# Kernel tuning notes

Hardware: AMD Instinct MI355X
Metric: run time of the kernel (lower is better)

Reference implementation:

```python
import jax, jax.numpy as jnp
import numpy as np

D_KQ = 1024  # output_key_query_dim, used for the 1/sqrt(d) scale


def setup_inputs() -> dict:
    key = jax.random.key(0)
    kx, kq, kk, kv = jax.random.split(key, 4)
    B, S, D = 4, 2048, 1024
    x = jax.random.normal(kx, (B, S, D), dtype=jnp.float32)
    # nn.Linear(in, out, bias=False) weights, shape (out, in); y = x @ W.T
    scale = 1.0 / np.sqrt(D)
    Wq = jax.random.normal(kq, (D_KQ, D), dtype=jnp.float32) * scale
    Wk = jax.random.normal(kk, (D_KQ, D), dtype=jnp.float32) * scale
    Wv = jax.random.normal(kv, (D, D), dtype=jnp.float32) * scale
    return {"x": x, "Wq": Wq, "Wk": Wk, "Wv": Wv}


def reference(x, Wq, Wk, Wv):
    # q, k, v projections (bias=False): y = x @ W.T
    q = jnp.einsum('bsd,ed->bse', x, Wq)  # [B,S,Dkq]
    k = jnp.einsum('bsd,ed->bse', x, Wk)  # [B,S,Dkq]
    v = jnp.einsum('bsd,ed->bse', x, Wv)  # [B,S,Dv]
    scores = jnp.einsum('bqe,bke->bqk', q, k) / jnp.sqrt(
        jnp.asarray(D_KQ, dtype=q.dtype))
    # NOTE: the original torch code's masked_fill(causal_mask == 1, -inf) is a
    # no-op because the buffer contains only {-inf, 0} values, never 1.
    # Faithfully, NO causal mask is applied.
    attn = jax.nn.softmax(scores, axis=-1)
    # dropout in eval mode -> identity
    out = jnp.einsum('bqk,bke->bqe', attn, v)  # [B,S,Dv]
    return out
```

## Files before the change

### kernel.cpp

```cpp
#include <hip/hip_runtime.h>
#include <stdint.h>

#define B_ 4
#define S_ 2048
#define D_ 1024

typedef __attribute__((ext_vector_type(8))) short short8;
typedef __attribute__((ext_vector_type(4))) float f32x4;
typedef __attribute__((ext_vector_type(4))) int int4v;

__device__ inline ushort f2bf(float f) {
  union { float f; uint32_t u; } v; v.f = f;
  uint32_t u = v.u;
  u += 0x7FFFu + ((u >> 16) & 1u);
  return (ushort)(u >> 16);
}

__device__ inline void gload_lds16(const ushort* g, ushort* l) {
  __builtin_amdgcn_global_load_lds(
      (__attribute__((address_space(1))) void*)(uintptr_t)g,
      (__attribute__((address_space(3))) void*)(uintptr_t)l,
      16, 0, 0);
}

__device__ inline uint lds_off(const ushort* p) {
  return (uint)(uintptr_t)(const __attribute__((address_space(3))) ushort*)(uintptr_t)p;
}

__device__ inline short8 dsr128(uint addr) {
  int4v r;
  asm volatile("ds_read_b128 %0, %1" : "=v"(r) : "v"(addr));
  return __builtin_bit_cast(short8, r);
}

__device__ inline void vwaitN(int n) {
  switch (n) {
    case 0: asm volatile("s_waitcnt vmcnt(0)"); break;
    case 1: asm volatile("s_waitcnt vmcnt(1)"); break;
    case 2: asm volatile("s_waitcnt vmcnt(2)"); break;
    case 3: asm volatile("s_waitcnt vmcnt(3)"); break;
    case 4: asm volatile("s_waitcnt vmcnt(4)"); break;
    case 5: asm volatile("s_waitcnt vmcnt(5)"); break;
    case 6: asm volatile("s_waitcnt vmcnt(6)"); break;
    case 7: asm volatile("s_waitcnt vmcnt(7)"); break;
    default: asm volatile("s_waitcnt vmcnt(8)"); break;
  }
}

__device__ inline void abar() { asm volatile("s_barrier"); }

__device__ inline void lgkm0() {
  asm volatile("s_waitcnt lgkmcnt(0)");
  __builtin_amdgcn_sched_barrier(0);
}

__global__ __launch_bounds__(256) void convert_all(
    const float* __restrict__ x, const float* __restrict__ wq,
    const float* __restrict__ wk, const float* __restrict__ wv,
    ushort* __restrict__ xb, ushort* __restrict__ wcat) {
  const int NX = B_ * S_ * D_;
  const int NW = D_ * D_;
  int e = (blockIdx.x * 256 + threadIdx.x) * 4;
  const float* src;
  ushort* dst;
  if (e < NX) {
    src = x + e; dst = xb + e;
  } else {
    int e2 = e - NX;
    int w = e2 / NW, off = e2 - w * NW;
    src = (w == 0 ? wq : w == 1 ? wk : wv) + off;
    dst = wcat + e2;
  }
  float4 f = *(const float4*)src;
  ushort4 o;
  o.x = f2bf(f.x); o.y = f2bf(f.y); o.z = f2bf(f.z); o.w = f2bf(f.w);
  *(ushort4*)dst = o;
}

template <int HH, int NH>
__device__ inline void mfma16(short8 (&af)[4][2], short8 (&bf)[2][2][2],
                              f32x4 (&acc)[8][4]) {
  __builtin_amdgcn_s_setprio(1);
  #pragma unroll
  for (int mf = 0; mf < 4; ++mf)
    #pragma unroll
    for (int nf = 0; nf < 2; ++nf)
      #pragma unroll
      for (int ks = 0; ks < 2; ++ks)
        acc[HH * 4 + mf][NH * 2 + nf] = __builtin_amdgcn_mfma_f32_16x16x32_bf16(
            af[mf][ks], bf[NH][nf][ks], acc[HH * 4 + mf][NH * 2 + nf], 0, 0, 0);
  __builtin_amdgcn_s_setprio(0);
}

template <bool SM>
__global__ __launch_bounds__(512, 2) void gemm256(
    const ushort* __restrict__ A, const ushort* __restrict__ Bm,
    ushort* __restrict__ C, float* __restrict__ psum,
    int K, int lda, int ldb, int ldc,
    long sA, long sB, long sC, float scale) {
  constexpr int ATILE = 256 * 64;
  __shared__ ushort lds[4 * ATILE];
  ushort* ldsA = lds;
  ushort* ldsB = lds + 2 * ATILE;

  const int tid = threadIdx.x;
  const int wid = tid >> 6, lane = tid & 63;
  const int wr = wid >> 2, wc = wid & 3;
  const int la = lane & 15, kg = lane >> 4;
  const int m0 = blockIdx.x * 256, n0 = blockIdx.y * 256;
  const int bz = blockIdx.z;
  const ushort* Ag = A + (size_t)bz * sA;
  const ushort* Bg = Bm + (size_t)bz * sB;

  uint aOff[2][2]; int aDst[2][2];
  uint bOff[2][2]; int bDst[2][2];
  #pragma unroll
  for (int h = 0; h < 2; ++h)
    #pragma unroll
    for (int l = 0; l < 2; ++l) {
      int li = l * 512 + tid, ridx = li >> 3, c = li & 7;
      int rowA = (ridx < 64) ? h * 64 + ridx : 128 + h * 64 + (ridx - 64);
      int gcA = c ^ (rowA & 7);
      aOff[h][l] = (uint)((m0 + rowA) * lda + gcA * 8);
      aDst[h][l] = rowA * 64 + c * 8;
      int rowB = (ridx >> 5) * 64 + h * 32 + (ridx & 31);
      int gcB = c ^ (rowB & 7);
      bOff[h][l] = (uint)((n0 + rowB) * ldb + gcB * 8);
      bDst[h][l] = rowB * 64 + c * 8;
    }

  auto stageA = [&](int h, int buf, int t) {
    #pragma unroll
    for (int l = 0; l < 2; ++l)
      gload_lds16(Ag + aOff[h][l] + (size_t)t * 64, ldsA + buf * ATILE + aDst[h][l]);
  };
  auto stageB = [&](int h, int buf, int t) {
    #pragma unroll
    for (int l = 0; l < 2; ++l)
      gload_lds16(Bg + bOff[h][l] + (size_t)t * 64, ldsB + buf * ATILE + bDst[h][l]);
  };

  uint offAq[2][2][4];
  #pragma unroll
  for (int hh = 0; hh < 2; ++hh)
    #pragma unroll
    for (int ks = 0; ks < 2; ++ks)
      #pragma unroll
      for (int mf = 0; mf < 4; ++mf) {
        int row = wr * 128 + hh * 64 + mf * 16 + la;
        int kc = ((ks * 4 + kg) ^ (row & 7)) * 8;
        offAq[hh][ks][mf] = (uint)((row * 64 + kc) * 2);
      }
  uint offBq[2][2][2];
  #pragma unroll
  for (int nh = 0; nh < 2; ++nh)
    #pragma unroll
    for (int ks = 0; ks < 2; ++ks)
      #pragma unroll
      for (int nf = 0; nf < 2; ++nf) {
        int row = wc * 64 + nh * 32 + nf * 16 + la;
        int kc = ((ks * 4 + kg) ^ (row & 7)) * 8;
        offBq[nh][ks][nf] = (uint)((row * 64 + kc) * 2);
      }
  const uint ldsA0 = lds_off(ldsA);
  const uint ldsB0 = lds_off(ldsB);

  f32x4 acc[8][4];
  #pragma unroll
  for (int m = 0; m < 8; ++m)
    #pragma unroll
    for (int n = 0; n < 4; ++n) acc[m][n] = (f32x4)(0.f);
  short8 af[4][2];
  short8 bf[2][2][2];

  const int NT = K / 64;

  stageA(0, 0, 0); stageB(0, 0, 0); stageB(1, 0, 0); stageA(1, 0, 0);

  for (int t = 0; t < NT; ++t) {
    const uint aB = ldsA0 + (uint)((t & 1) * ATILE * 2);
    const uint bB = ldsB0 + (uint)((t & 1) * ATILE * 2);
    const int nb = (t + 1) & 1;

    vwaitN(4);
    abar();
    #pragma unroll
    for (int mf = 0; mf < 4; ++mf)
      #pragma unroll
      for (int ks = 0; ks < 2; ++ks) af[mf][ks] = dsr128(aB + offAq[0][ks][mf]);
    #pragma unroll
    for (int nf = 0; nf < 2; ++nf)
      #pragma unroll
      for (int ks = 0; ks < 2; ++ks) bf[0][nf][ks] = dsr128(bB + offBq[0][ks][nf]);
    if (t + 1 < NT) stageA(0, nb, t + 1);
    lgkm0();
    mfma16<0, 0>(af, bf, acc);

    vwaitN(t + 1 < NT ? 4 : 2);
    abar();
    #pragma unroll
    for (int nf = 0; nf < 2; ++nf)
      #pragma unroll
      for (int ks = 0; ks < 2; ++ks) bf[1][nf][ks] = dsr128(bB + offBq[1][ks][nf]);
    if (t + 1 < NT) stageB(0, nb, t + 1);
    lgkm0();
    mfma16<0, 1>(af, bf, acc);

    vwaitN(t + 1 < NT ? 4 : 0);
    abar();
    #pragma unroll
    for (int mf = 0; mf < 4; ++mf)
      #pragma unroll
      for (int ks = 0; ks < 2; ++ks) af[mf][ks] = dsr128(aB + offAq[1][ks][mf]);
    if (t + 1 < NT) stageB(1, nb, t + 1);
    lgkm0();
    mfma16<1, 0>(af, bf, acc);

    if (t + 1 < NT) stageA(1, nb, t + 1);
    mfma16<1, 1>(af, bf, acc);
  }

  if constexpr (SM) {
    __shared__ float psum_lds[4][256];
    float rsum[8][4];
    #pragma unroll
    for (int mf = 0; mf < 8; ++mf)
      #pragma unroll
      for (int jj = 0; jj < 4; ++jj) rsum[mf][jj] = 0.f;
    #pragma unroll
    for (int mf = 0; mf < 8; ++mf) {
      #pragma unroll
      for (int nf = 0; nf < 4; ++nf) {
        int r = m0 + wr * 128 + (mf >> 2) * 64 + (mf & 3) * 16 + kg * 4;
        int col = n0 + wc * 64 + (nf >> 1) * 32 + (nf & 1) * 16 + la;
        #pragma unroll
        for (int jj = 0; jj < 4; ++jj) {
          float e = __expf(acc[mf][nf][jj] * scale);
          C[(size_t)bz * sC + (size_t)(r + jj) * ldc + col] = f2bf(e);
          rsum[mf][jj] += e;
        }
      }
    }
    #pragma unroll
    for (int mf = 0; mf < 8; ++mf)
      #pragma unroll
      for (int jj = 0; jj < 4; ++jj) {
        float s = rsum[mf][jj];
        s += __shfl_xor(s, 1); s += __shfl_xor(s, 2);
        s += __shfl_xor(s, 4); s += __shfl_xor(s, 8);
        if (la == 0)
          psum_lds[wc][wr * 128 + (mf >> 2) * 64 + (mf & 3) * 16 + kg * 4 + jj] = s;
      }
    __syncthreads();
    if (tid < 256)
      psum[((size_t)bz * 8 + blockIdx.y) * 2048 + m0 + tid] =
          psum_lds[0][tid] + psum_lds[1][tid] + psum_lds[2][tid] + psum_lds[3][tid];
  } else {
    #pragma unroll
    for (int mf = 0; mf < 8; ++mf) {
      #pragma unroll
      for (int nf = 0; nf < 4; ++nf) {
        int r = m0 + wr * 128 + (mf >> 2) * 64 + (mf & 3) * 16 + kg * 4;
        int col = n0 + wc * 64 + (nf >> 1) * 32 + (nf & 1) * 16 + la;
        #pragma unroll
        for (int jj = 0; jj < 4; ++jj)
          C[(size_t)bz * sC + (size_t)(r + jj) * ldc + col] =
              f2bf(acc[mf][nf][jj] * scale);
      }
    }
  }
}

template <int H, int BM, int BN>
__device__ inline void mfma_ph(short8 (&afv)[BM / 64], short8 (&bfv)[BN / 64],
                               f32x4 (&acc)[BM / 32][BN / 64]) {
  constexpr int J = BM / 64, NF = BN / 64;
  __builtin_amdgcn_s_setprio(1);
  #pragma unroll
  for (int j = 0; j < J; ++j)
    #pragma unroll
    for (int nf = 0; nf < NF; ++nf)
      acc[H * J + j][nf] = __builtin_amdgcn_mfma_f32_16x16x32_bf16(
          afv[j], bfv[nf], acc[H * J + j][nf], 0, 0, 0);
  __builtin_amdgcn_s_setprio(0);
}

template <int BM, int BN, bool OUT_BF16, bool V_TRANS, bool NORM>
__global__ __launch_bounds__(512, 2) void gemm_p(
    const ushort* __restrict__ A, const ushort* __restrict__ Bm,
    void* __restrict__ C, ushort* __restrict__ Vt,
    const float* __restrict__ psum,
    int N, int K, int lda, int ldb, int ldc,
    long sA, long sB, long sC, float scale) {
  constexpr int J = BM / 64, NF = BN / 64, MF = BM / 32;
  constexpr int LAH = BM / 128;
  constexpr int LBH = BN / 128;
  constexpr int ABUF = BM * 64;
  constexpr int BBUF = BN * 64;
  constexpr int VW1 = 2 * LAH + 2 * LBH;
  __shared__ ushort lds[2 * ABUF + 3 * BBUF];
  ushort* ldsA = lds;
  ushort* ldsB = lds + 2 * ABUF;

  const int tid = threadIdx.x;
  const int wid = tid >> 6, lane = tid & 63;
  const int wr = wid >> 2, wc = wid & 3;
  const int la = lane & 15, kg = lane >> 4;
  const int m0 = blockIdx.x * BM, n0 = blockIdx.y * BN;
  const int bz = blockIdx.z;
  const ushort* Ag = A + (size_t)bz * sA;
  const ushort* Bg = Bm + (size_t)bz * sB;

  uint aOff[2][LAH]; int aDst[2][LAH];
  #pragma unroll
  for (int h = 0; h < 2; ++h)
    #pragma unroll
    for (int l = 0; l < LAH; ++l) {
      int li = l * 512 + tid, ridx = li >> 3, c = li & 7;
      int row = (ridx < BM / 4) ? h * (BM / 4) + ridx
                                : (h + 2) * (BM / 4) + (ridx - BM / 4);
      int gc = c ^ (row & 7);
      aOff[h][l] = (uint)((m0 + row) * lda + gc * 8);
      aDst[h][l] = row * 64 + c * 8;
    }
  uint bOff[2][LBH]; int bDst[2][LBH];
  #pragma unroll
  for (int h = 0; h < 2; ++h)
    #pragma unroll
    for (int l = 0; l < LBH; ++l) {
      int li = l * 512 + tid, ridx = li >> 3, c = li & 7;
      int row = h * (BN / 2) + ridx;
      int gc = c ^ (row & 7);
      bOff[h][l] = (uint)((n0 + row) * ldb + gc * 8);
      bDst[h][l] = row * 64 + c * 8;
    }

  auto stageA = [&](int h, int buf, int t) {
    #pragma unroll
    for (int l = 0; l < LAH; ++l)
      gload_lds16(Ag + aOff[h][l] + (size_t)t * 64, ldsA + buf * ABUF + aDst[h][l]);
  };
  auto stageB = [&](int h, int slot, int t) {
    #pragma unroll
    for (int l = 0; l < LBH; ++l)
      gload_lds16(Bg + bOff[h][l] + (size_t)t * 64, ldsB + slot * BBUF + bDst[h][l]);
  };

  uint offA[2][2][J];
  #pragma unroll
  for (int h = 0; h < 2; ++h)
    #pragma unroll
    for (int ks = 0; ks < 2; ++ks)
      #pragma unroll
      for (int j = 0; j < J; ++j) {
        int row = wr * (BM / 2) + h * (BM / 4) + j * 16 + la;
        int kc = ((ks * 4 + kg) ^ (row & 7)) * 8;
        offA[h][ks][j] = (uint)((row * 64 + kc) * 2);
      }
  uint offB[2][NF];
  #pragma unroll
  for (int ks = 0; ks < 2; ++ks)
    #pragma unroll
    for (int nf = 0; nf < NF; ++nf) {
      int row = wc * (BN / 4) + nf * 16 + la;
      int kc = ((ks * 4 + kg) ^ (row & 7)) * 8;
      offB[ks][nf] = (uint)((row * 64 + kc) * 2);
    }
  const uint ldsA0 = lds_off(ldsA);
  const uint ldsB0 = lds_off(ldsB);

  f32x4 acc[MF][NF];
  #pragma unroll
  for (int m = 0; m < MF; ++m)
    #pragma unroll
    for (int n = 0; n < NF; ++n) acc[m][n] = (f32x4)(0.f);
  short8 af[J], bf0[NF], bf1[NF];

  const int NT = K / 64;

  stageA(0, 0, 0); stageB(0, 0, 0); stageB(1, 0, 0);
  stageA(1, 0, 0);
  stageA(0, 1, 1); stageB(0, 1, 1); stageB(1, 1, 1);

  int bs = 0;
  for (int t = 0; t < NT; ++t) {
    const uint aB = ldsA0 + (uint)((t & 1) * ABUF * 2);
    const uint bB = ldsB0 + (uint)(bs * BBUF * 2);
    const int bs2 = (bs == 0) ? 2 : bs - 1;

    vwaitN(t + 1 < NT ? VW1 : LAH);
    abar();
    #pragma unroll
    for (int j = 0; j < J; ++j) af[j] = dsr128(aB + offA[0][0][j]);
    #pragma unroll
    for (int nf = 0; nf < NF; ++nf) bf0[nf] = dsr128(bB + offB[0][nf]);
    if (t + 1 < NT) stageA(1, (t + 1) & 1, t + 1);
    lgkm0();
    mfma_ph<0, BM, BN>(af, bf0, acc);
    #pragma unroll
    for (int j = 0; j < J; ++j) af[j] = dsr128(aB + offA[0][1][j]);
    #pragma unroll
    for (int nf = 0; nf < NF; ++nf) bf1[nf] = dsr128(bB + offB[1][nf]);
    lgkm0();
    mfma_ph<0, BM, BN>(af, bf1, acc);

    vwaitN(t + 1 < NT ? VW1 : 0);
    abar();
    #pragma unroll
    for (int j = 0; j < J; ++j) af[j] = dsr128(aB + offA[1][0][j]);
    if (t + 2 < NT) { stageA(0, t & 1, t + 2); stageB(0, bs2, t + 2); }
    lgkm0();
    mfma_ph<1, BM, BN>(af, bf0, acc);
    #pragma unroll
    for (int j = 0; j < J; ++j) af[j] = dsr128(aB + offA[1][1][j]);
    if (t + 2 < NT) stageB(1, bs2, t + 2);
    lgkm0();
    mfma_ph<1, BM, BN>(af, bf1, acc);

    bs = (bs == 2) ? 0 : bs + 1;
  }

  __shared__ float inv_l[BM];
  if constexpr (NORM) {
    __syncthreads();
    if (tid < BM) {
      float s = 0.f;
      #pragma unroll
      for (int q = 0; q < 8; ++q)
        s += psum[((size_t)bz * 8 + q) * 2048 + m0 + tid];
      inv_l[tid] = 1.0f / s;
    }
    __syncthreads();
  }

  if constexpr (V_TRANS) {
    const int b = m0 >> 11;
    ushort* Vb = Vt + (size_t)b * D_ * S_;
    #pragma unroll
    for (int m = 0; m < MF; ++m) {
      #pragma unroll
      for (int n = 0; n < NF; ++n) {
        int r = m0 + wr * (BM / 2) + m * 16 + kg * 4;
        int e = n0 + wc * (BN / 4) + n * 16 + la;
        int s0 = r & 2047;
        ushort4 o;
        o.x = f2bf(acc[m][n][0]); o.y = f2bf(acc[m][n][1]);
        o.z = f2bf(acc[m][n][2]); o.w = f2bf(acc[m][n][3]);
        *(ushort4*)&Vb[(size_t)e * S_ + s0] = o;
      }
    }
  } else {
    char* Cb = (char*)C;
    #pragma unroll
    for (int m = 0; m < MF; ++m) {
      #pragma unroll
      for (int n = 0; n < NF; ++n) {
        int rl = wr * (BM / 2) + m * 16 + kg * 4;
        int col = n0 + wc * (BN / 4) + n * 16 + la;
        #pragma unroll
        for (int jj = 0; jj < 4; ++jj) {
          float sc = NORM ? inv_l[rl + jj] : scale;
          float v = acc[m][n][jj] * sc;
          size_t idx = (size_t)bz * sC + (size_t)(m0 + rl + jj) * ldc + col;
          if (OUT_BF16) ((ushort*)Cb)[idx] = f2bf(v);
          else          ((float*)Cb)[idx]  = v;
        }
      }
    }
  }
}

extern "C" void kernel_launch(void* const* d_in, const int* in_sizes, int n_in,
                              void* d_out, int out_size, void* d_ws, size_t ws_size,
                              hipStream_t stream) {
  const float* x  = (const float*)d_in[0];
  const float* Wq = (const float*)d_in[1];
  const float* Wk = (const float*)d_in[2];
  const float* Wv = (const float*)d_in[3];
  float* out = (float*)d_out;

  char* ws = (char*)d_ws;
  ushort* Xb   = (ushort*)(ws + 0);
  ushort* Wcat = (ushort*)(ws + 16777216);
  ushort* QKV  = (ushort*)(ws + 23068672);
  ushort* Vt   = (ushort*)(ws + 73400320);
  ushort* Pu   = (ushort*)(ws + 90177536);
  float*  psum = (float*) (ws + 157286400);

  const int NTOT = B_ * S_ * D_ + 3 * D_ * D_;

  convert_all<<<NTOT / 4 / 256, 256, 0, stream>>>(x, Wq, Wk, Wv, Xb, Wcat);

  gemm256<false><<<dim3(32, 8, 1), 512, 0, stream>>>(
      Xb, Wcat, QKV, nullptr, 1024, 1024, 1024, 3072, 0, 0, 0, 1.0f);

  gemm_p<128, 256, true, true, false><<<dim3(64, 4, 1), 512, 0, stream>>>(
      Xb, Wcat + (size_t)2048 * 1024, nullptr, Vt, nullptr,
      1024, 1024, 1024, 1024, 0, 0, 0, 0, 1.0f);

  gemm256<true><<<dim3(8, 8, B_), 512, 0, stream>>>(
      QKV, QKV + 1024, Pu, psum, 1024, 3072, 3072, 2048,
      (long)S_ * 3072, (long)S_ * 3072, (long)S_ * S_, 1.0f / 32.0f);

  gemm_p<128, 256, false, false, true><<<dim3(16, 4, B_), 512, 0, stream>>>(
      Pu, Vt, out, nullptr, psum, 1024, 2048, 2048, 2048, 1024,
      (long)S_ * S_, (long)S_ * D_, (long)S_ * D_, 1.0f);
}
```

Measured before the change: 156.5 us.

## Replace gemm_p with 256x128 tiled qgemm using double-buffered A/B staging

Replaces the templated 128x256 gemm_p kernel with a fixed 256x128 tile kernel used for the V projection and the P·V GEMM. The B-operand staging moves from a triple-buffered ring that loaded two K-steps ahead to plain double buffering that loads one step ahead. A and B fragments for both k-substeps are now loaded together before each MFMA phase. The taller M tile and narrower N tile change the per-block operand reuse ratio and halve the number of blocks in the M dimension. The shallower prefetch risks exposing more global-load latency.

```diff
diff --git a/kernel.cpp b/kernel.cpp
--- a/kernel.cpp
+++ b/kernel.cpp
@@ -271,159 +271,143 @@
   }
 }
 
-template <int H, int BM, int BN>
-__device__ inline void mfma_ph(short8 (&afv)[BM / 64], short8 (&bfv)[BN / 64],
-                               f32x4 (&acc)[BM / 32][BN / 64]) {
-  constexpr int J = BM / 64, NF = BN / 64;
+template <int HH>
+__device__ inline void mfma16n(short8 (&af)[4][2], short8 (&bf)[2][2],
+                               f32x4 (&acc)[8][2]) {
   __builtin_amdgcn_s_setprio(1);
   #pragma unroll
-  for (int j = 0; j < J; ++j)
-    #pragma unroll
-    for (int nf = 0; nf < NF; ++nf)
-      acc[H * J + j][nf] = __builtin_amdgcn_mfma_f32_16x16x32_bf16(
-          afv[j], bfv[nf], acc[H * J + j][nf], 0, 0, 0);
+  for (int mf = 0; mf < 4; ++mf)
+    #pragma unroll
+    for (int nf = 0; nf < 2; ++nf)
+      #pragma unroll
+      for (int ks = 0; ks < 2; ++ks)
+        acc[HH * 4 + mf][nf] = __builtin_amdgcn_mfma_f32_16x16x32_bf16(
+            af[mf][ks], bf[nf][ks], acc[HH * 4 + mf][nf], 0, 0, 0);
   __builtin_amdgcn_s_setprio(0);
 }
 
-template <int BM, int BN, bool OUT_BF16, bool V_TRANS, bool NORM>
-__global__ __launch_bounds__(512, 2) void gemm_p(
+template <bool V_TRANS, bool NORM>
+__global__ __launch_bounds__(512, 2) void qgemm(
     const ushort* __restrict__ A, const ushort* __restrict__ Bm,
-    void* __restrict__ C, ushort* __restrict__ Vt,
+    float* __restrict__ C, ushort* __restrict__ Vt,
     const float* __restrict__ psum,
-    int N, int K, int lda, int ldb, int ldc,
-    long sA, long sB, long sC, float scale) {
-  constexpr int J = BM / 64, NF = BN / 64, MF = BM / 32;
-  constexpr int LAH = BM / 128;
-  constexpr int LBH = BN / 128;
-  constexpr int ABUF = BM * 64;
-  constexpr int BBUF = BN * 64;
-  constexpr int VW1 = 2 * LAH + 2 * LBH;
-  __shared__ ushort lds[2 * ABUF + 3 * BBUF];
+    int K, int lda, int ldb, int ldc,
+    long sA, long sB, long sC) {
+  constexpr int ATILE = 256 * 64;
+  constexpr int BTILE = 128 * 64;
+  __shared__ ushort lds[2 * ATILE + 2 * BTILE];
   ushort* ldsA = lds;
-  ushort* ldsB = lds + 2 * ABUF;
+  ushort* ldsB = lds + 2 * ATILE;
 
   const int tid = threadIdx.x;
   const int wid = tid >> 6, lane = tid & 63;
   const int wr = wid >> 2, wc = wid & 3;
   const int la = lane & 15, kg = lane >> 4;
-  const int m0 = blockIdx.x * BM, n0 = blockIdx.y * BN;
+  const int m0 = blockIdx.x * 256, n0 = blockIdx.y * 128;
   const int bz = blockIdx.z;
   const ushort* Ag = A + (size_t)bz * sA;
   const ushort* Bg = Bm + (size_t)bz * sB;
 
-  uint aOff[2][LAH]; int aDst[2][LAH];
+  uint aOff[2][2]; int aDst[2][2];
   #pragma unroll
   for (int h = 0; h < 2; ++h)
     #pragma unroll
-    for (int l = 0; l < LAH; ++l) {
+    for (int l = 0; l < 2; ++l) {
       int li = l * 512 + tid, ridx = li >> 3, c = li & 7;
-      int row = (ridx < BM / 4) ? h * (BM / 4) + ridx
-                                : (h + 2) * (BM / 4) + (ridx - BM / 4);
-      int gc = c ^ (row & 7);
-      aOff[h][l] = (uint)((m0 + row) * lda + gc * 8);
-      aDst[h][l] = row * 64 + c * 8;
-    }
-  uint bOff[2][LBH]; int bDst[2][LBH];
-  #pragma unroll
-  for (int h = 0; h < 2; ++h)
-    #pragma unroll
-    for (int l = 0; l < LBH; ++l) {
-      int li = l * 512 + tid, ridx = li >> 3, c = li & 7;
-      int row = h * (BN / 2) + ridx;
-      int gc = c ^ (row & 7);
-      bOff[h][l] = (uint)((n0 + row) * ldb + gc * 8);
-      bDst[h][l] = row * 64 + c * 8;
-    }
+      int rowA = (ridx < 64) ? h * 64 + ridx : 128 + h * 64 + (ridx - 64);
+      int gcA = c ^ (rowA & 7);
+      aOff[h][l] = (uint)((m0 + rowA) * lda + gcA * 8);
+      aDst[h][l] = rowA * 64 + c * 8;
+    }
+  uint bOff[2]; int bDst[2];
+  #pragma unroll
+  for (int l = 0; l < 2; ++l) {
+    int li = l * 512 + tid, ridx = li >> 3, c = li & 7;
+    int gcB = c ^ (ridx & 7);
+    bOff[l] = (uint)((n0 + ridx) * ldb + gcB * 8);
+    bDst[l] = ridx * 64 + c * 8;
+  }
 
   auto stageA = [&](int h, int buf, int t) {
     #pragma unroll
-    for (int l = 0; l < LAH; ++l)
-      gload_lds16(Ag + aOff[h][l] + (size_t)t * 64, ldsA + buf * ABUF + aDst[h][l]);
+    for (int l = 0; l < 2; ++l)
+      gload_lds16(Ag + aOff[h][l] + (size_t)t * 64, ldsA + buf * ATILE + aDst[h][l]);
   };
-  auto stageB = [&](int h, int slot, int t) {
-    #pragma unroll
-    for (int l = 0; l < LBH; ++l)
-      gload_lds16(Bg + bOff[h][l] + (size_t)t * 64, ldsB + slot * BBUF + bDst[h][l]);
+  auto stageB = [&](int buf, int t) {
+    #pragma unroll
+    for (int l = 0; l < 2; ++l)
+      gload_lds16(Bg + bOff[l] + (size_t)t * 64, ldsB + buf * BTILE + bDst[l]);
   };
 
-  uint offA[2][2][J];
-  #pragma unroll
-  for (int h = 0; h < 2; ++h)
+  uint offAq[2][2][4];
+  #pragma unroll
+  for (int hh = 0; hh < 2; ++hh)
     #pragma unroll
     for (int ks = 0; ks < 2; ++ks)
       #pragma unroll
-      for (int j = 0; j < J; ++j) {
-        int row = wr * (BM / 2) + h * (BM / 4) + j * 16 + la;
+      for (int mf = 0; mf < 4; ++mf) {
+        int row = wr * 128 + hh * 64 + mf * 16 + la;
         int kc = ((ks * 4 + kg) ^ (row & 7)) * 8;
-        offA[h][ks][j] = (uint)((row * 64 + kc) * 2);
-      }
-  uint offB[2][NF];
+        offAq[hh][ks][mf] = (uint)((row * 64 + kc) * 2);
+      }
+  uint offBq[2][2];
   #pragma unroll
   for (int ks = 0; ks < 2; ++ks)
     #pragma unroll
-    for (int nf = 0; nf < NF; ++nf) {
-      int row = wc * (BN / 4) + nf * 16 + la;
+    for (int nf = 0; nf < 2; ++nf) {
+      int row = wc * 32 + nf * 16 + la;
       int kc = ((ks * 4 + kg) ^ (row & 7)) * 8;
-      offB[ks][nf] = (uint)((row * 64 + kc) * 2);
+      offBq[ks][nf] = (uint)((row * 64 + kc) * 2);
     }
   const uint ldsA0 = lds_off(ldsA);
   const uint ldsB0 = lds_off(ldsB);
 
-  f32x4 acc[MF][NF];
-  #pragma unroll
-  for (int m = 0; m < MF; ++m)
-    #pragma unroll
-    for (int n = 0; n < NF; ++n) acc[m][n] = (f32x4)(0.f);
-  short8 af[J], bf0[NF], bf1[NF];
+  f32x4 acc[8][2];
+  #pragma unroll
+  for (int m = 0; m < 8; ++m)
+    #pragma unroll
+    for (int n = 0; n < 2; ++n) acc[m][n] = (f32x4)(0.f);
+  short8 af[4][2];
+  short8 bf[2][2];
 
   const int NT = K / 64;
 
-  stageA(0, 0, 0); stageB(0, 0, 0); stageB(1, 0, 0);
-  stageA(1, 0, 0);
-  stageA(0, 1, 1); stageB(0, 1, 1); stageB(1, 1, 1);
-
-  int bs = 0;
+  stageA(0, 0, 0); stageB(0, 0); stageA(1, 0, 0);
+
   for (int t = 0; t < NT; ++t) {
-    const uint aB = ldsA0 + (uint)((t & 1) * ABUF * 2);
-    const uint bB = ldsB0 + (uint)(bs * BBUF * 2);
-    const int bs2 = (bs == 0) ? 2 : bs - 1;
-
-    vwaitN(t + 1 < NT ? VW1 : LAH);
+    const uint aB = ldsA0 + (uint)((t & 1) * ATILE * 2);
+    const uint bB = ldsB0 + (uint)((t & 1) * BTILE * 2);
+    const int nb = (t + 1) & 1;
+
+    vwaitN(2);
     abar();
     #pragma unroll
-    for (int j = 0; j < J; ++j) af[j] = dsr128(aB + offA[0][0][j]);
-    #pragma unroll
-    for (int nf = 0; nf < NF; ++nf) bf0[nf] = dsr128(bB + offB[0][nf]);
-    if (t + 1 < NT) stageA(1, (t + 1) & 1, t + 1);
+    for (int mf = 0; mf < 4; ++mf)
+      #pragma unroll
+      for (int ks = 0; ks < 2; ++ks) af[mf][ks] = dsr128(aB + offAq[0][ks][mf]);
+    #pragma unroll
+    for (int nf = 0; nf < 2; ++nf)
+      #pragma unroll
+      for (int ks = 0; ks < 2; ++ks) bf[nf][ks] = dsr128(bB + offBq[ks][nf]);
+    if (t + 1 < NT) { stageA(0, nb, t + 1); stageB(nb, t + 1); }
     lgkm0();
-    mfma_ph<0, BM, BN>(af, bf0, acc);
-    #pragma unroll
-    for (int j = 0; j < J; ++j) af[j] = dsr128(aB + offA[0][1][j]);
-    #pragma unroll
-    for (int nf = 0; nf < NF; ++nf) bf1[nf] = dsr128(bB + offB[1][nf]);
+    mfma16n<0>(af, bf, acc);
+
+    vwaitN(t + 1 < NT ? 4 : 0);
+    abar();
+    #pragma unroll
+    for (int mf = 0; mf < 4; ++mf)
+      #pragma unroll
+      for (int ks = 0; ks < 2; ++ks) af[mf][ks] = dsr128(aB + offAq[1][ks][mf]);
+    if (t + 1 < NT) stageA(1, nb, t + 1);
     lgkm0();
-    mfma_ph<0, BM, BN>(af, bf1, acc);
-
-    vwaitN(t + 1 < NT ? VW1 : 0);
-    abar();
-    #pragma unroll
-    for (int j = 0; j < J; ++j) af[j] = dsr128(aB + offA[1][0][j]);
-    if (t + 2 < NT) { stageA(0, t & 1, t + 2); stageB(0, bs2, t + 2); }
-    lgkm0();
-    mfma_ph<1, BM, BN>(af, bf0, acc);
-    #pragma unroll
-    for (int j = 0; j < J; ++j) af[j] = dsr128(aB + offA[1][1][j]);
-    if (t + 2 < NT) stageB(1, bs2, t + 2);
-    lgkm0();
-    mfma_ph<1, BM, BN>(af, bf1, acc);
-
-    bs = (bs == 2) ? 0 : bs + 1;
-  }
-
-  __shared__ float inv_l[BM];
+    mfma16n<1>(af, bf, acc);
+  }
+
+  __shared__ float inv_l[256];
   if constexpr (NORM) {
     __syncthreads();
-    if (tid < BM) {
+    if (tid < 256) {
       float s = 0.f;
       #pragma unroll
       for (int q = 0; q < 8; ++q)
@@ -437,33 +421,30 @@
     const int b = m0 >> 11;
     ushort* Vb = Vt + (size_t)b * D_ * S_;
     #pragma unroll
-    for (int m = 0; m < MF; ++m) {
-      #pragma unroll
-      for (int n = 0; n < NF; ++n) {
-        int r = m0 + wr * (BM / 2) + m * 16 + kg * 4;
-        int e = n0 + wc * (BN / 4) + n * 16 + la;
+    for (int mf = 0; mf < 8; ++mf) {
+      #pragma unroll
+      for (int nf = 0; nf < 2; ++nf) {
+        int r = m0 + wr * 128 + (mf >> 2) * 64 + (mf & 3) * 16 + kg * 4;
+        int e = n0 + wc * 32 + nf * 16 + la;
         int s0 = r & 2047;
         ushort4 o;
-        o.x = f2bf(acc[m][n][0]); o.y = f2bf(acc[m][n][1]);
-        o.z = f2bf(acc[m][n][2]); o.w = f2bf(acc[m][n][3]);
+        o.x = f2bf(acc[mf][nf][0]); o.y = f2bf(acc[mf][nf][1]);
+        o.z = f2bf(acc[mf][nf][2]); o.w = f2bf(acc[mf][nf][3]);
         *(ushort4*)&Vb[(size_t)e * S_ + s0] = o;
       }
     }
   } else {
-    char* Cb = (char*)C;
-    #pragma unroll
-    for (int m = 0; m < MF; ++m) {
-      #pragma unroll
-      for (int n = 0; n < NF; ++n) {
-        int rl = wr * (BM / 2) + m * 16 + kg * 4;
-        int col = n0 + wc * (BN / 4) + n * 16 + la;
+    #pragma unroll
+    for (int mf = 0; mf < 8; ++mf) {
+      #pragma unroll
+      for (int nf = 0; nf < 2; ++nf) {
+        int rl = wr * 128 + (mf >> 2) * 64 + (mf & 3) * 16 + kg * 4;
+        int col = n0 + wc * 32 + nf * 16 + la;
         #pragma unroll
         for (int jj = 0; jj < 4; ++jj) {
-          float sc = NORM ? inv_l[rl + jj] : scale;
-          float v = acc[m][n][jj] * sc;
-          size_t idx = (size_t)bz * sC + (size_t)(m0 + rl + jj) * ldc + col;
-          if (OUT_BF16) ((ushort*)Cb)[idx] = f2bf(v);
-          else          ((float*)Cb)[idx]  = v;
+          float sc = NORM ? inv_l[rl + jj] : 1.0f;
+          C[(size_t)bz * sC + (size_t)(m0 + rl + jj) * ldc + col] =
+              acc[mf][nf][jj] * sc;
         }
       }
     }
@@ -494,15 +475,15 @@
   gemm256<false><<<dim3(32, 8, 1), 512, 0, stream>>>(
       Xb, Wcat, QKV, nullptr, 1024, 1024, 1024, 3072, 0, 0, 0, 1.0f);
 
-  gemm_p<128, 256, true, true, false><<<dim3(64, 4, 1), 512, 0, stream>>>(
+  qgemm<true, false><<<dim3(32, 8, 1), 512, 0, stream>>>(
       Xb, Wcat + (size_t)2048 * 1024, nullptr, Vt, nullptr,
-      1024, 1024, 1024, 1024, 0, 0, 0, 0, 1.0f);
+      1024, 1024, 1024, 1024, 0, 0, 0);
 
   gemm256<true><<<dim3(8, 8, B_), 512, 0, stream>>>(
       QKV, QKV + 1024, Pu, psum, 1024, 3072, 3072, 2048,
       (long)S_ * 3072, (long)S_ * 3072, (long)S_ * S_, 1.0f / 32.0f);
 
-  gemm_p<128, 256, false, false, true><<<dim3(16, 4, B_), 512, 0, stream>>>(
-      Pu, Vt, out, nullptr, psum, 1024, 2048, 2048, 2048, 1024,
-      (long)S_ * S_, (long)S_ * D_, (long)S_ * D_, 1.0f);
-}
+  qgemm<false, true><<<dim3(8, 8, B_), 512, 0, stream>>>(
+      Pu, Vt, out, nullptr, psum, 2048, 2048, 2048, 1024,
+      (long)S_ * S_, (long)D_ * S_, (long)S_ * D_);
+}
```

Result: no change. 155.5 us (-0.7%).
